# Optimization experiments

Measured on AMD Instinct MI355X. Metric: run time of the kernel, lower is better.

## Reference

```python
import jax, jax.numpy as jnp
import numpy as np

B, S, D = 2, 2048, 1024
H, KS, VS = 16, 64, 64

def setup_inputs() -> dict:
    key = jax.random.key(0)
    ks = jax.random.split(key, 11)
    s = 1.0 / np.sqrt(D)
    return {
        "query": jax.random.normal(ks[0], (B, S, D), jnp.float32),
        "key":   jax.random.normal(ks[1], (B, S, D), jnp.float32),
        "value": jax.random.normal(ks[2], (B, S, D), jnp.float32),
        # weights stored [in, out] (transpose of torch Linear)
        "Wq": jax.random.normal(ks[3], (D, H * KS), jnp.float32) * s,
        "bq": jnp.zeros((H * KS,), jnp.float32),
        "Wk": jax.random.normal(ks[4], (D, H * KS), jnp.float32) * s,
        "bk": jnp.zeros((H * KS,), jnp.float32),
        "Wv": jax.random.normal(ks[5], (D, H * VS), jnp.float32) * s,
        "bv": jnp.zeros((H * VS,), jnp.float32),
        "Wo": jax.random.normal(ks[6], (H * VS, D), jnp.float32) * s,
        "bo": jnp.zeros((D,), jnp.float32),
    }

def reference(query, key, value, Wq, bq, Wk, bk, Wv, bv, Wo, bo):
    b = query.shape[0]
    # projections + split heads -> [B, H, S, d]
    Q = (query @ Wq + bq).reshape(b, -1, H, KS).transpose(0, 2, 1, 3)
    K = (key   @ Wk + bk).reshape(b, -1, H, KS).transpose(0, 2, 1, 3)
    V = (value @ Wv + bv).reshape(b, -1, H, VS).transpose(0, 2, 1, 3)
    scores = jnp.einsum('bhqd,bhkd->bhqk', Q, K) / jnp.sqrt(jnp.float32(KS))
    attn = jax.nn.softmax(scores, axis=-1)  # dropout_rate=0.0 -> identity
    ctx = jnp.einsum('bhqk,bhkd->bhqd', attn, V)  # [B,H,S,VS]
    ctx = ctx.transpose(0, 2, 1, 3).reshape(b, attn.shape[-1], H * VS)
    out = ctx @ Wo + bo
    return out, attn
```

## Files before the change

### kernel.cpp

```cpp
#include <hip/hip_runtime.h>
#include <stdint.h>


typedef _Float16 f16;
typedef f16 f16x4 __attribute__((ext_vector_type(4)));
typedef f16 f16x8 __attribute__((ext_vector_type(8)));
typedef float f32x4 __attribute__((ext_vector_type(4)));
typedef uint32_t u32;
typedef u32 u32x4 __attribute__((ext_vector_type(4)));

#define L2E 1.4426950408889634f

__device__ __forceinline__ void gload16(const void* g, void* l) {
    __builtin_amdgcn_global_load_lds((__attribute__((address_space(1))) void*)g,
                                     (__attribute__((address_space(3))) void*)l,
                                     16, 0, 0);
}

__global__ __launch_bounds__(256) void k_cvt(const float* __restrict__ q,
                                             const float* __restrict__ k,
                                             const float* __restrict__ v,
                                             f16* __restrict__ dst)
{
    int z = blockIdx.z;
    const float* s = (z == 0) ? q : (z == 1) ? k : v;
    size_t i = (size_t)blockIdx.x * 256 + threadIdx.x;
    float4 f = ((const float4*)s)[i];
    f16x4 o = {(f16)f.x, (f16)f.y, (f16)f.z, (f16)f.w};
    *(f16x4*)(dst + (size_t)z * 4194304 + i * 4) = o;
}

__global__ __launch_bounds__(256) void k_wtrans(const float* __restrict__ w0,
                                                const float* __restrict__ w1,
                                                const float* __restrict__ w2,
                                                const float* __restrict__ w3,
                                                f16* __restrict__ wt)
{
    __shared__ f16 t[64][72];
    int z = blockIdx.z;
    const float* W = (z == 0) ? w0 : (z == 1) ? w1 : (z == 2) ? w2 : w3;
    f16* outp = wt + (size_t)z * 1048576;
    int tx = blockIdx.x, ty = blockIdx.y, tid = threadIdx.x;
#pragma unroll
    for (int r4 = 0; r4 < 4; r4++) {
        int row = r4 * 16 + (tid >> 4);
        int col = (tid & 15) * 4;
        float4 f = *(const float4*)(W + (size_t)(ty * 64 + row) * 1024 + tx * 64 + col);
        t[col + 0][row] = (f16)f.x; t[col + 1][row] = (f16)f.y;
        t[col + 2][row] = (f16)f.z; t[col + 3][row] = (f16)f.w;
    }
    __syncthreads();
#pragma unroll
    for (int cc = 0; cc < 2; cc++) {
        int c = tid + cc * 256;
        int row = c >> 3, ch = c & 7;
        f16x8 vv;
#pragma unroll
        for (int j = 0; j < 8; j++) vv[j] = t[row][ch * 8 + j];
        *(f16x8*)(outp + (size_t)(tx * 64 + row) * 1024 + ty * 64 + ch * 8) = vv;
    }
}

__global__ __launch_bounds__(256) void k_gemm(const f16* __restrict__ Ab,
                                              const f16* __restrict__ Wtb,
                                              const float* __restrict__ b0,
                                              const float* __restrict__ b1,
                                              const float* __restrict__ b2,
                                              void* __restrict__ o0,
                                              void* __restrict__ o1,
                                              int proj)
{
    __shared__ __align__(16) char As[16384];
    __shared__ __align__(16) char Bs[16384];
    const int tid = threadIdx.x;
    const int wv = tid >> 6, ln = tid & 63, lg = ln >> 4, li = ln & 15;
    const int m0 = blockIdx.y * 128, n0 = blockIdx.x * 128;
    const int wm = (wv >> 1) * 64, wn = (wv & 1) * 64;

    const f16* A; const f16* Bt; const float* bias; int mode;
    if (proj) {
        int z = blockIdx.z;
        A = Ab + (size_t)z * 4194304;
        Bt = Wtb + (size_t)z * 1048576;
        bias = (z == 0) ? b0 : (z == 1) ? b1 : b2;
        mode = (z == 2) ? 1 : 0;
    } else { A = Ab; Bt = Wtb; bias = b0; mode = 2; }

    const char* gA[4]; const char* gB[4];
#pragma unroll
    for (int c = 0; c < 4; c++) {
        int r = (wv * 4 + c) * 8 + (ln >> 3);
        int j = (ln & 7) ^ (r & 7);
        gA[c] = (const char*)A  + (size_t)(m0 + r) * 2048 + j * 16;
        gB[c] = (const char*)Bt + (size_t)(n0 + r) * 2048 + j * 16;
    }

    f32x4 acc[4][4] = {};
    for (int kt = 0; kt < 16; kt++) {
        __syncthreads();
#pragma unroll
        for (int c = 0; c < 4; c++) {
            gload16(gA[c] + kt * 128, As + (wv * 4 + c) * 1024);
            gload16(gB[c] + kt * 128, Bs + (wv * 4 + c) * 1024);
        }
        __syncthreads();
#pragma unroll
        for (int kk = 0; kk < 2; kk++) {
            f16x8 af[4], bf[4];
#pragma unroll
            for (int mi = 0; mi < 4; mi++) {
                int row = wm + mi * 16 + li;
                af[mi] = *(const f16x8*)(As + row * 128 + (((kk * 4 + lg) ^ (row & 7)) * 16));
            }
#pragma unroll
            for (int ni = 0; ni < 4; ni++) {
                int row = wn + ni * 16 + li;
                bf[ni] = *(const f16x8*)(Bs + row * 128 + (((kk * 4 + lg) ^ (row & 7)) * 16));
            }
#pragma unroll
            for (int mi = 0; mi < 4; mi++)
#pragma unroll
                for (int ni = 0; ni < 4; ni++)
                    acc[mi][ni] = __builtin_amdgcn_mfma_f32_16x16x32_f16(af[mi], bf[ni], acc[mi][ni], 0, 0, 0);
        }
    }

    float bvs[4];
#pragma unroll
    for (int ni = 0; ni < 4; ni++) bvs[ni] = bias[n0 + wn + ni * 16 + li];

    if (mode == 2) {
        float* O = (float*)o0;
#pragma unroll
        for (int mi = 0; mi < 4; mi++)
#pragma unroll
            for (int ni = 0; ni < 4; ni++) {
                int n = n0 + wn + ni * 16 + li;
#pragma unroll
                for (int r = 0; r < 4; r++) {
                    int m = m0 + wm + mi * 16 + lg * 4 + r;
                    O[(size_t)m * 1024 + n] = acc[mi][ni][r] + bvs[ni];
                }
            }
    } else if (mode == 0) {
        f16* O = (f16*)o0 + (size_t)blockIdx.z * 4194304;
#pragma unroll
        for (int mi = 0; mi < 4; mi++)
#pragma unroll
            for (int ni = 0; ni < 4; ni++) {
                int n = n0 + wn + ni * 16 + li;
                int h = n >> 6, d = n & 63;
#pragma unroll
                for (int r = 0; r < 4; r++) {
                    int m = m0 + wm + mi * 16 + lg * 4 + r;
                    int b = m >> 11, s = m & 2047;
                    O[(((size_t)b * 16 + h) * 2048 + s) * 64 + d] = (f16)(acc[mi][ni][r] + bvs[ni]);
                }
            }
    } else {
        f16* O = (f16*)o1;
#pragma unroll
        for (int mi = 0; mi < 4; mi++)
#pragma unroll
            for (int ni = 0; ni < 4; ni++) {
                int n = n0 + wn + ni * 16 + li;
                int h = n >> 6, d = n & 63;
                int mb = m0 + wm + mi * 16 + lg * 4;
                int b = mb >> 11, s = mb & 2047;
                f16x4 pk;
#pragma unroll
                for (int r = 0; r < 4; r++) pk[r] = (f16)(acc[mi][ni][r] + bvs[ni]);
                *(f16x4*)(O + (((size_t)b * 16 + h) * 64 + d) * 2048 + s) = pk;
            }
    }
}

__global__ __launch_bounds__(256, 3) void k_attn(const f16* __restrict__ Qb,
                                                 const f16* __restrict__ Kb,
                                                 const f16* __restrict__ Vt,
                                                 float* __restrict__ attn,
                                                 f16* __restrict__ ctx)
{
    __shared__ __align__(16) char Ks[32768];
    __shared__ __align__(16) char Ps[4][2048];
    const int tid = threadIdx.x, wv = tid >> 6, ln = tid & 63, lg = ln >> 4, li = ln & 15;
    const int bid = blockIdx.x;
    const int kk = bid >> 3;
    const int bh = (bid & 7) * 4 + (kk >> 5);
    const int q0 = (kk & 31) * 64 + wv * 16;

    const char* KbB = (const char*)Kb + (size_t)bh * 262144;
    const char* VtB = (const char*)Vt + (size_t)bh * 262144;

    const f16* qrow = Qb + ((size_t)bh * 2048 + q0 + li) * 64 + lg * 8;
    f16x8 aq0 = *(const f16x8*)(qrow);
    f16x8 aq1 = *(const f16x8*)(qrow + 32);
#pragma unroll
    for (int j = 0; j < 8; j++) {
        aq0[j] = (f16)((float)aq0[j] * 0.125f);
        aq1[j] = (f16)((float)aq1[j] * 0.125f);
    }

    float lacc[4] = {0.f, 0.f, 0.f, 0.f};
    {
        int swp[4];
        const char* gp[4];
#pragma unroll
        for (int t = 0; t < 4; t++) {
            int c = tid + t * 256;
            int r = c >> 3, j = c & 7;
            swp[t] = r * 128 + ((j ^ (r & 7)) * 16);
            gp[t] = KbB + (size_t)r * 128 + j * 16;
        }
        u32x4 s[4];
#pragma unroll
        for (int t = 0; t < 4; t++) s[t] = *(const u32x4*)(gp[t]);
#pragma unroll
        for (int t = 0; t < 4; t++) *(u32x4*)(Ks + swp[t]) = s[t];
#pragma unroll
        for (int t = 0; t < 4; t++) s[t] = *(const u32x4*)(gp[t] + 16384);
        __syncthreads();
        for (int kt = 0; kt < 16; kt++) {
            const char* cur = Ks + (kt & 1) * 16384;
            if (kt + 1 < 16) {
                char* nxt = Ks + ((kt + 1) & 1) * 16384;
#pragma unroll
                for (int t = 0; t < 4; t++) *(u32x4*)(nxt + swp[t]) = s[t];
                if (kt + 2 < 16) {
#pragma unroll
                    for (int t = 0; t < 4; t++)
                        s[t] = *(const u32x4*)(gp[t] + (size_t)(kt + 2) * 16384);
                }
            }
#pragma unroll
            for (int cf = 0; cf < 8; cf++) {
                int row = cf * 16 + li;
                f16x8 ak0 = *(const f16x8*)(cur + row * 128 + ((lg ^ (row & 7)) * 16));
                f16x8 ak1 = *(const f16x8*)(cur + row * 128 + (((4 + lg) ^ (row & 7)) * 16));
                __builtin_amdgcn_s_setprio(1);
                f32x4 z = {0.f, 0.f, 0.f, 0.f};
                z = __builtin_amdgcn_mfma_f32_16x16x32_f16(ak0, aq0, z, 0, 0, 0);
                z = __builtin_amdgcn_mfma_f32_16x16x32_f16(ak1, aq1, z, 0, 0, 0);
                __builtin_amdgcn_s_setprio(0);
                lacc[cf & 3] += exp2f(z[0] * L2E) + exp2f(z[1] * L2E)
                              + exp2f(z[2] * L2E) + exp2f(z[3] * L2E);
            }
            if (kt + 1 < 16) __syncthreads();
        }
    }
    float l_ = (lacc[0] + lacc[1]) + (lacc[2] + lacc[3]);
    l_ += __shfl_xor(l_, 16);
    l_ += __shfl_xor(l_, 32);
    const float inv_l = 1.0f / l_;
    float* aRow = attn + ((size_t)bh * 2048 + q0 + li) * 2048;
    char* Pw = Ps[wv];

    __syncthreads();

    f32x4 cacc[4] = {};
    const int r0 = tid >> 3, j0 = tid & 7;
    const int r1 = (tid + 256) >> 3, j1 = (tid + 256) & 7;
    const int sw0 = r0 * 128 + ((j0 ^ (r0 & 7)) * 16);
    const int sw1 = r1 * 128 + ((j1 ^ (r1 & 7)) * 16);
    u32x4 sk0 = *(const u32x4*)(KbB + (size_t)r0 * 128 + j0 * 16);
    u32x4 sk1 = *(const u32x4*)(KbB + (size_t)r1 * 128 + j1 * 16);
    *(u32x4*)(Ks + sw0) = sk0;
    *(u32x4*)(Ks + sw1) = sk1;
    sk0 = *(const u32x4*)(KbB + (size_t)(64 + r0) * 128 + j0 * 16);
    sk1 = *(const u32x4*)(KbB + (size_t)(64 + r1) * 128 + j1 * 16);
    __syncthreads();
    for (int kt = 0; kt < 32; kt++) {
        const char* cur = Ks + (kt & 1) * 8192;
        if (kt + 1 < 32) {
            char* nxt = Ks + ((kt + 1) & 1) * 8192;
            *(u32x4*)(nxt + sw0) = sk0;
            *(u32x4*)(nxt + sw1) = sk1;
            if (kt + 2 < 32) {
                sk0 = *(const u32x4*)(KbB + (size_t)((kt + 2) * 64 + r0) * 128 + j0 * 16);
                sk1 = *(const u32x4*)(KbB + (size_t)((kt + 2) * 64 + r1) * 128 + j1 * 16);
            }
        }
        f16x8 vf[4][2];
#pragma unroll
        for (int df = 0; df < 4; df++) {
            const char* vr = VtB + (size_t)(df * 16 + li) * 4096 + kt * 128 + lg * 16;
            vf[df][0] = *(const f16x8*)vr;
            vf[df][1] = *(const f16x8*)(vr + 64);
        }
        f32x4 zz[4];
#pragma unroll
        for (int cf = 0; cf < 4; cf++) {
            int row = cf * 16 + li;
            f16x8 ak0 = *(const f16x8*)(cur + row * 128 + ((lg ^ (row & 7)) * 16));
            f16x8 ak1 = *(const f16x8*)(cur + row * 128 + (((4 + lg) ^ (row & 7)) * 16));
            __builtin_amdgcn_s_setprio(1);
            f32x4 z = {0.f, 0.f, 0.f, 0.f};
            z = __builtin_amdgcn_mfma_f32_16x16x32_f16(ak0, aq0, z, 0, 0, 0);
            z = __builtin_amdgcn_mfma_f32_16x16x32_f16(ak1, aq1, z, 0, 0, 0);
            __builtin_amdgcn_s_setprio(0);
            zz[cf] = z;
        }
#pragma unroll
        for (int cf = 0; cf < 4; cf++) {
            float p0 = exp2f(zz[cf][0] * L2E) * inv_l;
            float p1 = exp2f(zz[cf][1] * L2E) * inv_l;
            float p2 = exp2f(zz[cf][2] * L2E) * inv_l;
            float p3 = exp2f(zz[cf][3] * L2E) * inv_l;
            f32x4 fv = {p0, p1, p2, p3};
            __builtin_nontemporal_store(fv, (f32x4*)(aRow + kt * 64 + cf * 16 + lg * 4));
            f16x4 pk = {(f16)p0, (f16)p1, (f16)p2, (f16)p3};
            int c = cf * 2 + (lg >> 1);
            *(f16x4*)(Pw + li * 128 + ((c ^ (li & 7)) * 16) + (lg & 1) * 8) = pk;
        }
#pragma unroll
        for (int s2 = 0; s2 < 2; s2++) {
            f16x8 bp = *(const f16x8*)(Pw + li * 128 + (((s2 * 4 + lg) ^ (li & 7)) * 16));
            __builtin_amdgcn_s_setprio(1);
#pragma unroll
            for (int df = 0; df < 4; df++)
                cacc[df] = __builtin_amdgcn_mfma_f32_16x16x32_f16(vf[df][s2], bp, cacc[df], 0, 0, 0);
            __builtin_amdgcn_s_setprio(0);
        }
        if (kt + 1 < 32) __syncthreads();
    }

    const int b = bh >> 4, h = bh & 15;
#pragma unroll
    for (int df = 0; df < 4; df++) {
        f16x4 pk;
#pragma unroll
        for (int r = 0; r < 4; r++) pk[r] = (f16)cacc[df][r];
        size_t mrow = (size_t)b * 2048 + q0 + li;
        size_t n = (size_t)h * 64 + df * 16 + lg * 4;
        *(f16x4*)(ctx + mrow * 1024 + n) = pk;
    }
}

extern "C" void kernel_launch(void* const* d_in, const int* in_sizes, int n_in,
                              void* d_out, int out_size, void* d_ws, size_t ws_size,
                              hipStream_t stream)
{
    const float* q  = (const float*)d_in[0];
    const float* k  = (const float*)d_in[1];
    const float* v  = (const float*)d_in[2];
    const float* Wq = (const float*)d_in[3];
    const float* bq = (const float*)d_in[4];
    const float* Wk = (const float*)d_in[5];
    const float* bk = (const float*)d_in[6];
    const float* Wv = (const float*)d_in[7];
    const float* bv = (const float*)d_in[8];
    const float* Wo = (const float*)d_in[9];
    const float* bo = (const float*)d_in[10];

    f16* W = (f16*)d_ws;
    float* out = (float*)d_out;
    float* attn = out + 4194304;

    f16* X   = W;
    f16* Wt  = W + 12582912;
    f16* QKb = W + 16777216;
    f16* Vt  = W + 25165824;
    f16* ctx = W + 29360128;

    k_cvt<<<dim3(4096, 1, 3), 256, 0, stream>>>(q, k, v, X);
    k_wtrans<<<dim3(16, 16, 4), 256, 0, stream>>>(Wq, Wk, Wv, Wo, Wt);
    k_gemm<<<dim3(8, 32, 3), 256, 0, stream>>>(X, Wt, bq, bk, bv, QKb, Vt, 1);
    k_attn<<<dim3(1024), 256, 0, stream>>>(QKb, QKb + 4194304, Vt, attn, ctx);
    k_gemm<<<dim3(8, 32, 1), 256, 0, stream>>>(ctx, Wt + 3145728, bo, bo, bo, out, nullptr, 0);
}
```

Baseline: 277.7 us.

## Shrink K tiles, prefetch V one step ahead, use lightweight LDS barriers

The first pass (softmax denominator) now uses 64-row K tiles with a 16KB double buffer instead of 128-row tiles in 32KB, which cuts LDS use and may raise occupancy. The second pass is unrolled by two so the V fragments for the next tile load into registers while the current tile computes. __syncthreads is replaced by a barrier that waits only on LDS counters. The normalization is folded into the exponent as exp2(z*log2e - log2 l), removing a multiply. Risks are higher register pressure from the double V buffer and more barriers in the first pass.

After: 281.4 us. No clear change (+1.4%).

```diff
diff --git a/kernel.cpp b/kernel.cpp
--- a/kernel.cpp
+++ b/kernel.cpp
@@ -10,6 +10,12 @@
 typedef u32 u32x4 __attribute__((ext_vector_type(4)));
 
 #define L2E 1.4426950408889634f
+
+#define LDS_BARRIER() do { \
+    asm volatile("s_waitcnt lgkmcnt(0)" ::: "memory"); \
+    __builtin_amdgcn_sched_barrier(0); \
+    __builtin_amdgcn_s_barrier(); \
+} while (0)
 
 __device__ __forceinline__ void gload16(const void* g, void* l) {
     __builtin_amdgcn_global_load_lds((__attribute__((address_space(1))) void*)g,
@@ -181,7 +187,7 @@
                                                  float* __restrict__ attn,
                                                  f16* __restrict__ ctx)
 {
-    __shared__ __align__(16) char Ks[32768];
+    __shared__ __align__(16) char Ks[16384];
     __shared__ __align__(16) char Ps[4][2048];
     const int tid = threadIdx.x, wv = tid >> 6, ln = tid & 63, lg = ln >> 4, li = ln & 15;
     const int bid = blockIdx.x;
@@ -201,39 +207,33 @@
         aq1[j] = (f16)((float)aq1[j] * 0.125f);
     }
 
+    const int r0 = tid >> 3, j0 = tid & 7;
+    const int r1 = (tid + 256) >> 3, j1 = (tid + 256) & 7;
+    const int sw0 = r0 * 128 + ((j0 ^ (r0 & 7)) * 16);
+    const int sw1 = r1 * 128 + ((j1 ^ (r1 & 7)) * 16);
+
     float lacc[4] = {0.f, 0.f, 0.f, 0.f};
     {
-        int swp[4];
-        const char* gp[4];
-#pragma unroll
-        for (int t = 0; t < 4; t++) {
-            int c = tid + t * 256;
-            int r = c >> 3, j = c & 7;
-            swp[t] = r * 128 + ((j ^ (r & 7)) * 16);
-            gp[t] = KbB + (size_t)r * 128 + j * 16;
-        }
-        u32x4 s[4];
-#pragma unroll
-        for (int t = 0; t < 4; t++) s[t] = *(const u32x4*)(gp[t]);
-#pragma unroll
-        for (int t = 0; t < 4; t++) *(u32x4*)(Ks + swp[t]) = s[t];
-#pragma unroll
-        for (int t = 0; t < 4; t++) s[t] = *(const u32x4*)(gp[t] + 16384);
-        __syncthreads();
-        for (int kt = 0; kt < 16; kt++) {
-            const char* cur = Ks + (kt & 1) * 16384;
-            if (kt + 1 < 16) {
-                char* nxt = Ks + ((kt + 1) & 1) * 16384;
-#pragma unroll
-                for (int t = 0; t < 4; t++) *(u32x4*)(nxt + swp[t]) = s[t];
-                if (kt + 2 < 16) {
-#pragma unroll
-                    for (int t = 0; t < 4; t++)
-                        s[t] = *(const u32x4*)(gp[t] + (size_t)(kt + 2) * 16384);
+        u32x4 sk0 = *(const u32x4*)(KbB + (size_t)r0 * 128 + j0 * 16);
+        u32x4 sk1 = *(const u32x4*)(KbB + (size_t)r1 * 128 + j1 * 16);
+        *(u32x4*)(Ks + sw0) = sk0;
+        *(u32x4*)(Ks + sw1) = sk1;
+        sk0 = *(const u32x4*)(KbB + (size_t)(64 + r0) * 128 + j0 * 16);
+        sk1 = *(const u32x4*)(KbB + (size_t)(64 + r1) * 128 + j1 * 16);
+        LDS_BARRIER();
+        for (int kt = 0; kt < 32; kt++) {
+            const char* cur = Ks + (kt & 1) * 8192;
+            if (kt + 1 < 32) {
+                char* nxt = Ks + ((kt + 1) & 1) * 8192;
+                *(u32x4*)(nxt + sw0) = sk0;
+                *(u32x4*)(nxt + sw1) = sk1;
+                if (kt + 2 < 32) {
+                    sk0 = *(const u32x4*)(KbB + (size_t)((kt + 2) * 64 + r0) * 128 + j0 * 16);
+                    sk1 = *(const u32x4*)(KbB + (size_t)((kt + 2) * 64 + r1) * 128 + j1 * 16);
                 }
             }
 #pragma unroll
-            for (int cf = 0; cf < 8; cf++) {
+            for (int cf = 0; cf < 4; cf++) {
                 int row = cf * 16 + li;
                 f16x8 ak0 = *(const f16x8*)(cur + row * 128 + ((lg ^ (row & 7)) * 16));
                 f16x8 ak1 = *(const f16x8*)(cur + row * 128 + (((4 + lg) ^ (row & 7)) * 16));
@@ -242,87 +242,98 @@
                 z = __builtin_amdgcn_mfma_f32_16x16x32_f16(ak0, aq0, z, 0, 0, 0);
                 z = __builtin_amdgcn_mfma_f32_16x16x32_f16(ak1, aq1, z, 0, 0, 0);
                 __builtin_amdgcn_s_setprio(0);
-                lacc[cf & 3] += exp2f(z[0] * L2E) + exp2f(z[1] * L2E)
-                              + exp2f(z[2] * L2E) + exp2f(z[3] * L2E);
-            }
-            if (kt + 1 < 16) __syncthreads();
+                lacc[cf] += exp2f(z[0] * L2E) + exp2f(z[1] * L2E)
+                          + exp2f(z[2] * L2E) + exp2f(z[3] * L2E);
+            }
+            if (kt + 1 < 32) LDS_BARRIER();
         }
     }
     float l_ = (lacc[0] + lacc[1]) + (lacc[2] + lacc[3]);
     l_ += __shfl_xor(l_, 16);
     l_ += __shfl_xor(l_, 32);
-    const float inv_l = 1.0f / l_;
+    const float llog = -log2f(l_);
     float* aRow = attn + ((size_t)bh * 2048 + q0 + li) * 2048;
     char* Pw = Ps[wv];
 
-    __syncthreads();
-
     f32x4 cacc[4] = {};
-    const int r0 = tid >> 3, j0 = tid & 7;
-    const int r1 = (tid + 256) >> 3, j1 = (tid + 256) & 7;
-    const int sw0 = r0 * 128 + ((j0 ^ (r0 & 7)) * 16);
-    const int sw1 = r1 * 128 + ((j1 ^ (r1 & 7)) * 16);
+
+#define LOADV(buf, kt) do { \
+    _Pragma("unroll") for (int df = 0; df < 4; df++) { \
+        const char* vr = VtB + (size_t)(df * 16 + li) * 4096 + (kt) * 128 + lg * 16; \
+        buf[df][0] = *(const f16x8*)vr; \
+        buf[df][1] = *(const f16x8*)(vr + 64); \
+    } } while (0)
+
+#define STEP(kt, CUR, vbuf) do { \
+    f32x4 zz[4]; \
+    _Pragma("unroll") for (int cf = 0; cf < 4; cf++) { \
+        int row = cf * 16 + li; \
+        f16x8 ak0 = *(const f16x8*)((CUR) + row * 128 + ((lg ^ (row & 7)) * 16)); \
+        f16x8 ak1 = *(const f16x8*)((CUR) + row * 128 + (((4 + lg) ^ (row & 7)) * 16)); \
+        __builtin_amdgcn_s_setprio(1); \
+        f32x4 z = {0.f, 0.f, 0.f, 0.f}; \
+        z = __builtin_amdgcn_mfma_f32_16x16x32_f16(ak0, aq0, z, 0, 0, 0); \
+        z = __builtin_amdgcn_mfma_f32_16x16x32_f16(ak1, aq1, z, 0, 0, 0); \
+        __builtin_amdgcn_s_setprio(0); \
+        zz[cf] = z; \
+    } \
+    _Pragma("unroll") for (int cf = 0; cf < 4; cf++) { \
+        float p0 = exp2f(fmaf(zz[cf][0], L2E, llog)); \
+        float p1 = exp2f(fmaf(zz[cf][1], L2E, llog)); \
+        float p2 = exp2f(fmaf(zz[cf][2], L2E, llog)); \
+        float p3 = exp2f(fmaf(zz[cf][3], L2E, llog)); \
+        f32x4 fv = {p0, p1, p2, p3}; \
+        __builtin_nontemporal_store(fv, (f32x4*)(aRow + (kt) * 64 + cf * 16 + lg * 4)); \
+        f16x4 pk = {(f16)p0, (f16)p1, (f16)p2, (f16)p3}; \
+        int c = cf * 2 + (lg >> 1); \
+        *(f16x4*)(Pw + li * 128 + ((c ^ (li & 7)) * 16) + (lg & 1) * 8) = pk; \
+    } \
+    _Pragma("unroll") for (int s2 = 0; s2 < 2; s2++) { \
+        f16x8 bp = *(const f16x8*)(Pw + li * 128 + (((s2 * 4 + lg) ^ (li & 7)) * 16)); \
+        __builtin_amdgcn_s_setprio(1); \
+        _Pragma("unroll") for (int df = 0; df < 4; df++) \
+            cacc[df] = __builtin_amdgcn_mfma_f32_16x16x32_f16(vbuf[df][s2], bp, cacc[df], 0, 0, 0); \
+        __builtin_amdgcn_s_setprio(0); \
+    } } while (0)
+
     u32x4 sk0 = *(const u32x4*)(KbB + (size_t)r0 * 128 + j0 * 16);
     u32x4 sk1 = *(const u32x4*)(KbB + (size_t)r1 * 128 + j1 * 16);
+    f16x8 vfA[4][2], vfB[4][2];
+    LDS_BARRIER();
     *(u32x4*)(Ks + sw0) = sk0;
     *(u32x4*)(Ks + sw1) = sk1;
     sk0 = *(const u32x4*)(KbB + (size_t)(64 + r0) * 128 + j0 * 16);
     sk1 = *(const u32x4*)(KbB + (size_t)(64 + r1) * 128 + j1 * 16);
-    __syncthreads();
-    for (int kt = 0; kt < 32; kt++) {
-        const char* cur = Ks + (kt & 1) * 8192;
-        if (kt + 1 < 32) {
-            char* nxt = Ks + ((kt + 1) & 1) * 8192;
+    LOADV(vfA, 0);
+    LDS_BARRIER();
+
+    for (int t = 0; t < 16; t++) {
+        {
+            char* nxt = Ks + 8192;
             *(u32x4*)(nxt + sw0) = sk0;
             *(u32x4*)(nxt + sw1) = sk1;
-            if (kt + 2 < 32) {
-                sk0 = *(const u32x4*)(KbB + (size_t)((kt + 2) * 64 + r0) * 128 + j0 * 16);
-                sk1 = *(const u32x4*)(KbB + (size_t)((kt + 2) * 64 + r1) * 128 + j1 * 16);
-            }
-        }
-        f16x8 vf[4][2];
-#pragma unroll
-        for (int df = 0; df < 4; df++) {
-            const char* vr = VtB + (size_t)(df * 16 + li) * 4096 + kt * 128 + lg * 16;
-            vf[df][0] = *(const f16x8*)vr;
-            vf[df][1] = *(const f16x8*)(vr + 64);
-        }
-        f32x4 zz[4];
-#pragma unroll
-        for (int cf = 0; cf < 4; cf++) {
-            int row = cf * 16 + li;
-            f16x8 ak0 = *(const f16x8*)(cur + row * 128 + ((lg ^ (row & 7)) * 16));
-            f16x8 ak1 = *(const f16x8*)(cur + row * 128 + (((4 + lg) ^ (row & 7)) * 16));
-            __builtin_amdgcn_s_setprio(1);
-            f32x4 z = {0.f, 0.f, 0.f, 0.f};
-            z = __builtin_amdgcn_mfma_f32_16x16x32_f16(ak0, aq0, z, 0, 0, 0);
-            z = __builtin_amdgcn_mfma_f32_16x16x32_f16(ak1, aq1, z, 0, 0, 0);
-            __builtin_amdgcn_s_setprio(0);
-            zz[cf] = z;
-        }
-#pragma unroll
-        for (int cf = 0; cf < 4; cf++) {
-            float p0 = exp2f(zz[cf][0] * L2E) * inv_l;
-            float p1 = exp2f(zz[cf][1] * L2E) * inv_l;
-            float p2 = exp2f(zz[cf][2] * L2E) * inv_l;
-            float p3 = exp2f(zz[cf][3] * L2E) * inv_l;
-            f32x4 fv = {p0, p1, p2, p3};
-            __builtin_nontemporal_store(fv, (f32x4*)(aRow + kt * 64 + cf * 16 + lg * 4));
-            f16x4 pk = {(f16)p0, (f16)p1, (f16)p2, (f16)p3};
-            int c = cf * 2 + (lg >> 1);
-            *(f16x4*)(Pw + li * 128 + ((c ^ (li & 7)) * 16) + (lg & 1) * 8) = pk;
-        }
-#pragma unroll
-        for (int s2 = 0; s2 < 2; s2++) {
-            f16x8 bp = *(const f16x8*)(Pw + li * 128 + (((s2 * 4 + lg) ^ (li & 7)) * 16));
-            __builtin_amdgcn_s_setprio(1);
-#pragma unroll
-            for (int df = 0; df < 4; df++)
-                cacc[df] = __builtin_amdgcn_mfma_f32_16x16x32_f16(vf[df][s2], bp, cacc[df], 0, 0, 0);
-            __builtin_amdgcn_s_setprio(0);
-        }
-        if (kt + 1 < 32) __syncthreads();
-    }
+            if (t < 15) {
+                sk0 = *(const u32x4*)(KbB + (size_t)((2 * t + 2) * 64 + r0) * 128 + j0 * 16);
+                sk1 = *(const u32x4*)(KbB + (size_t)((2 * t + 2) * 64 + r1) * 128 + j1 * 16);
+            }
+            LOADV(vfB, 2 * t + 1);
+            STEP(2 * t, Ks, vfA);
+            LDS_BARRIER();
+        }
+        {
+            if (t < 15) {
+                *(u32x4*)(Ks + sw0) = sk0;
+                *(u32x4*)(Ks + sw1) = sk1;
+                sk0 = *(const u32x4*)(KbB + (size_t)((2 * t + 3) * 64 + r0) * 128 + j0 * 16);
+                sk1 = *(const u32x4*)(KbB + (size_t)((2 * t + 3) * 64 + r1) * 128 + j1 * 16);
+                LOADV(vfA, 2 * t + 2);
+            }
+            STEP(2 * t + 1, (const char*)(Ks + 8192), vfB);
+            if (t < 15) LDS_BARRIER();
+        }
+    }
+#undef LOADV
+#undef STEP
 
     const int b = bh >> 4, h = bh & 15;
 #pragma unroll
```
